# Kernel optimization log

Measured on AMD Instinct MI355X. Metric: run time of the kernel, lower is better.

Reference implementation:

```python
import jax, jax.numpy as jnp
import numpy as np

EMBED_DIM = 1024
NUM_HEADS = 16
HEAD_DIM = EMBED_DIM // NUM_HEADS
ROPE_BASE = 10000.0


def rotate_half(x):
    d = x.shape[-1] // 2
    x1, x2 = x[..., :d], x[..., d:]
    return jnp.concatenate((-x2, x1), axis=-1)


def setup_inputs() -> dict:
    key = jax.random.key(0)
    k_x, k_wqkv, k_bqkv, k_wo, k_bo = jax.random.split(key, 5)
    C = EMBED_DIM
    x = jax.random.normal(k_x, (4, 2048, C), dtype=jnp.float32)
    s = 1.0 / np.sqrt(C)
    W_qkv = jax.random.uniform(k_wqkv, (C, 3 * C), minval=-s, maxval=s, dtype=jnp.float32)
    b_qkv = jax.random.uniform(k_bqkv, (3 * C,), minval=-s, maxval=s, dtype=jnp.float32)
    W_out = jax.random.uniform(k_wo, (C, C), minval=-s, maxval=s, dtype=jnp.float32)
    b_out = jax.random.uniform(k_bo, (C,), minval=-s, maxval=s, dtype=jnp.float32)
    return {"x": x, "W_qkv": W_qkv, "b_qkv": b_qkv, "W_out": W_out, "b_out": b_out}


def reference(x, W_qkv, b_qkv, W_out, b_out):
    B, T, C = x.shape
    H, Dh = NUM_HEADS, HEAD_DIM
    # fused QKV projection: [B,T,3C] -> [3,B,H,T,Dh]
    qkv = (x @ W_qkv + b_qkv).reshape(B, T, 3, H, Dh).transpose(2, 0, 3, 1, 4)
    q, k, v = qkv[0], qkv[1], qkv[2]
    # rotary embedding: freqs [T, Dh/2] -> emb [T, Dh]
    inv_freq = 1.0 / (ROPE_BASE ** (jnp.arange(0, Dh, 2, dtype=jnp.float32) / Dh))
    freqs = jnp.arange(T, dtype=jnp.float32)[:, None] * inv_freq[None, :]
    emb = jnp.concatenate((freqs, freqs), axis=-1)  # [T, Dh], broadcasts over B,H
    cos, sin = jnp.cos(emb), jnp.sin(emb)
    q = q * cos + rotate_half(q) * sin
    k = k * cos + rotate_half(k) * sin
    # full (non-causal) attention, manual softmax
    scale = 1.0 / np.sqrt(Dh)
    attn = jax.nn.softmax(jnp.einsum("bhqd,bhkd->bhqk", q, k) * scale, axis=-1)
    out = jnp.einsum("bhqk,bhkd->bhqd", attn, v)  # [B,H,T,Dh]
    out = out.transpose(0, 2, 1, 3).reshape(B, T, C)
    return out @ W_out + b_out
```

## Files before the change

### kernel.cpp

```cpp
#include <hip/hip_runtime.h>
#include <math.h>

#define T_SEQ 2048
#define CDIM  1024
#define NH    16
#define DHD   64
#define BATCH 4
#define MROWS (BATCH * T_SEQ)
#define BHN   (BATCH * NH)

typedef _Float16 f16;
typedef __attribute__((ext_vector_type(8))) _Float16 f16x8;
typedef __attribute__((ext_vector_type(4))) _Float16 f16x4;
typedef __attribute__((ext_vector_type(2))) _Float16 f16x2;
typedef __attribute__((ext_vector_type(2))) __fp16 fp16x2;
typedef __attribute__((ext_vector_type(4))) float f32x4;

__device__ __forceinline__ float fast_exp2(float x) {
#if __has_builtin(__builtin_amdgcn_exp2f)
    return __builtin_amdgcn_exp2f(x);
#else
    return exp2f(x);
#endif
}

__device__ __forceinline__ float fast_rcp(float x) {
#if __has_builtin(__builtin_amdgcn_rcpf)
    return __builtin_amdgcn_rcpf(x);
#else
    return 1.0f / x;
#endif
}

__device__ __forceinline__ f16x2 cvt_pk_f16(float a, float b) {
    fp16x2 r = __builtin_amdgcn_cvt_pkrtz(a, b);
    return __builtin_bit_cast(f16x2, r);
}

__device__ __forceinline__ void gl_lds16(const f16* g, f16* l) {
    __builtin_amdgcn_global_load_lds(
        (const __attribute__((address_space(1))) void*)(g),
        (__attribute__((address_space(3))) void*)(l),
        16, 0, 0);
}

__global__ void rope_tables_kernel(float* __restrict__ ctab, float* __restrict__ stab)
{
    int idx = blockIdx.x * 256 + threadIdx.x;
    int t = idx >> 5, i = idx & 31;
    double inv = pow(10000.0, -(double)(2 * i) / 64.0);
    double a = (double)t * inv;
    ctab[idx] = (float)cos(a);
    stab[idx] = (float)sin(a);
}

__global__ __launch_bounds__(256) void xcvt_kernel(
    const float* __restrict__ X, f16* __restrict__ Xf)
{
    int idx = blockIdx.x * 256 + threadIdx.x;
    const float4* src = (const float4*)X + (size_t)idx * 2;
    float4 a = src[0], b = src[1];
    f16x8 o;
    o[0] = (f16)a.x; o[1] = (f16)a.y; o[2] = (f16)a.z; o[3] = (f16)a.w;
    o[4] = (f16)b.x; o[5] = (f16)b.y; o[6] = (f16)b.z; o[7] = (f16)b.w;
    *((f16x8*)Xf + idx) = o;
}

__global__ __launch_bounds__(64) void wcvt_kernel(
    const float* __restrict__ Wq, const float* __restrict__ Wo,
    f16* __restrict__ Wqt, f16* __restrict__ Wot)
{
    int lane = threadIdx.x;
    int k0 = blockIdx.x * 8;
    int ny = blockIdx.y;
    const float* W;
    f16* Wt;
    int N, n;
    if (ny < 48) { W = Wq; Wt = Wqt; N = 3072; n = ny * 64 + lane; }
    else         { W = Wo; Wt = Wot; N = 1024; n = (ny - 48) * 64 + lane; }
    f16x8 o;
#pragma unroll
    for (int j = 0; j < 8; j++) o[j] = (f16)W[(size_t)(k0 + j) * N + n];
    *(f16x8*)(Wt + (size_t)n * CDIM + k0) = o;
}

#define GEMM_MAINLOOP(Aimg, Bimg, M0, N0)                                         \
    __shared__ f16 As[128][64], Bs[128][64];                                      \
    const int tid = threadIdx.x, wave = tid >> 6, lane = tid & 63;                \
    const int l16 = lane & 15, quad = lane >> 4;                                  \
    const int wm = wave >> 1, wn = wave & 1;                                      \
    f32x4 acc[4][4];                                                              \
    _Pragma("unroll") for (int i = 0; i < 4; i++)                                 \
        _Pragma("unroll") for (int j = 0; j < 4; j++)                             \
            acc[i][j] = (f32x4){0.f, 0.f, 0.f, 0.f};                              \
    const f16* sbase = (wave < 2) ? (Aimg) : (Bimg);                              \
    f16* lbase = ((wave < 2) ? &As[0][0] : &Bs[0][0]) + (wave & 1) * 4096;        \
    const size_t srow0 = ((wave < 2) ? (size_t)(M0) : (size_t)(N0)) + (wave & 1) * 64; \
    const int srow = lane >> 3, schunk = lane & 7;                                \
    const int gchunk = (schunk ^ srow) << 3;         \
    for (int k0 = 0; k0 < CDIM; k0 += 64) {                                       \
        _Pragma("unroll") for (int it = 0; it < 8; it++)                          \
            gl_lds16(sbase + (srow0 + it * 8 + srow) * CDIM + k0 + gchunk,        \
                     lbase + it * 512);                                           \
        __syncthreads();                                                          \
        _Pragma("unroll") for (int ks = 0; ks < 2; ks++) {                        \
            f16x8 fa[4], fb[4];                                                   \
            _Pragma("unroll") for (int mi = 0; mi < 4; mi++)                      \
                fa[mi] = *(const f16x8*)                                          \
                    &As[wm * 64 + mi * 16 + l16][((ks * 4 + quad) ^ (l16 & 7)) << 3]; \
            _Pragma("unroll") for (int ni = 0; ni < 4; ni++)                      \
                fb[ni] = *(const f16x8*)                                          \
                    &Bs[wn * 64 + ni * 16 + l16][((ks * 4 + quad) ^ (l16 & 7)) << 3]; \
            _Pragma("unroll") for (int mi = 0; mi < 4; mi++)                      \
                _Pragma("unroll") for (int ni = 0; ni < 4; ni++)                  \
                    acc[mi][ni] = __builtin_amdgcn_mfma_f32_16x16x32_f16(         \
                        fa[mi], fb[ni], acc[mi][ni], 0, 0, 0);                    \
        }                                                                         \
        __syncthreads();                                                          \
    }

__global__ __launch_bounds__(256) void qkv_gemm_kernel(
    const f16* __restrict__ Xf, const f16* __restrict__ Wt,
    const float* __restrict__ bias,
    const float* __restrict__ ctab, const float* __restrict__ stab,
    f16* __restrict__ qf, f16* __restrict__ kf, f16* __restrict__ vtb)
{
    const int m0 = blockIdx.x * 128;
    const int n0 = blockIdx.y * 128;
    GEMM_MAINLOOP(Xf, Wt, m0, n0)

    const int ncol0 = n0 + wn * 64;
    const int w = ncol0 >> 10;
    const int h = (ncol0 >> 6) & 15;
    const int b = m0 >> 11;
    const int trow0 = (m0 & 2047) + wm * 64 + quad * 4;
    float bia[4];
#pragma unroll
    for (int ni = 0; ni < 4; ni++) bia[ni] = bias[ncol0 + ni * 16 + l16];

    if (w < 2) {
        f16* oq = w ? kf : qf;
        const float sc = w ? 1.0f : 0.18033688011112042f;
#pragma unroll
        for (int mi = 0; mi < 4; mi++) {
#pragma unroll
            for (int i = 0; i < 4; i++) {
                int t = trow0 + mi * 16 + i;
                size_t rowoff = ((size_t)(b * NH + h) * T_SEQ + t) * DHD;
#pragma unroll
                for (int np = 0; np < 2; np++) {
                    int d = np * 16 + l16;
                    float v0 = acc[mi][np][i] + bia[np];
                    float v1 = acc[mi][np + 2][i] + bia[np + 2];
                    float c = ctab[(t << 5) + d];
                    float s = stab[(t << 5) + d];
                    oq[rowoff + d]      = (f16)((v0 * c - v1 * s) * sc);
                    oq[rowoff + d + 32] = (f16)((v1 * c + v0 * s) * sc);
                }
            }
        }
    } else {
#pragma unroll
        for (int mi = 0; mi < 4; mi++) {
            const int tb = trow0 + mi * 16;
#pragma unroll
            for (int ni = 0; ni < 4; ni++) {
                const int d = ni * 16 + l16;
                f16x4 pv;
#pragma unroll
                for (int i = 0; i < 4; i++) pv[i] = (f16)(acc[mi][ni][i] + bia[ni]);
                *(f16x4*)(vtb + ((size_t)(b * NH + h) * DHD + d) * T_SEQ + tb) = pv;
            }
        }
    }
}

__global__ __launch_bounds__(256, 4) void attn_kernel(
    const f16* __restrict__ qf, const f16* __restrict__ kf,
    const f16* __restrict__ vt, f16* __restrict__ ab)
{
    __shared__ f16 Kb[2][64][64];
    __shared__ f16 Vb[2][64][64];
    __shared__ f16 Pb[4][32][32];

    const int tid  = threadIdx.x;
    const int wave = tid >> 6, lane = tid & 63;
    const int l16  = lane & 15, quad = lane >> 4;

    const int flat = blockIdx.x + (blockIdx.y << 4);
    const int swz  = (flat & 7) * 128 + (flat >> 3);
    const int qt = swz & 15;
    const int bh = swz >> 4;
    const int q0 = qt * 128 + wave * 32;

    const f16* kbase = kf + (size_t)bh * T_SEQ * DHD;
    const f16* vbase = vt + (size_t)bh * DHD * T_SEQ;

    f16x8 qfr[2][2];
#pragma unroll
    for (int qs = 0; qs < 2; qs++) {
        const f16* qrow = qf + ((size_t)bh * T_SEQ + q0 + qs * 16 + l16) * DHD;
        qfr[qs][0] = *(const f16x8*)(qrow + quad * 8);
        qfr[qs][1] = *(const f16x8*)(qrow + 32 + quad * 8);
    }

    f32x4 o[2][4];
    f32x4 lacc[2];
#pragma unroll
    for (int qs = 0; qs < 2; qs++) {
        lacc[qs] = (f32x4){0.f, 0.f, 0.f, 0.f};
#pragma unroll
        for (int dt = 0; dt < 4; dt++) o[qs][dt] = (f32x4){0.f, 0.f, 0.f, 0.f};
    }
    f16x8 ones;
#pragma unroll
    for (int j = 0; j < 8; j++) ones[j] = (f16)1.0f;

    const int srow = tid >> 3;
    const int scw  = tid & 7;
    const int scol = scw << 3;
    const int swzc = (scw ^ (srow & 7)) << 3;

    const int prot = l16 & 14;

    const f16* kp = kbase + (size_t)srow * DHD + scol;
    const f16* vp = vbase + (size_t)srow * T_SEQ + scol;

    f16x8 kreg[2], vreg[2];
#pragma unroll
    for (int r = 0; r < 2; r++) {
        kreg[r] = *(const f16x8*)(kp + (size_t)(r * 32) * DHD);
        vreg[r] = *(const f16x8*)(vp + (size_t)(r * 32) * T_SEQ);
    }
#pragma unroll
    for (int r = 0; r < 2; r++) {
        *(f16x8*)&Kb[0][srow + r * 32][swzc] = kreg[r];
        *(f16x8*)&Vb[0][srow + r * 32][swzc] = vreg[r];
    }
    const f16* kq = kp + 64 * DHD;
    const f16* vq = vp + 64;
    __syncthreads();

    for (int kt = 0; kt < 32; kt++) {
        const int buf = kt & 1;
        if (kt < 31) {
#pragma unroll
            for (int r = 0; r < 2; r++) {
                kreg[r] = *(const f16x8*)(kq + (size_t)(r * 32) * DHD);
                vreg[r] = *(const f16x8*)(vq + (size_t)(r * 32) * T_SEQ);
            }
            kq += 64 * DHD;
            vq += 64;
        }

#pragma unroll
        for (int half = 0; half < 2; half++) {
            f32x4 sc[2][2];
#pragma unroll
            for (int k2 = 0; k2 < 2; k2++)
#pragma unroll
                for (int qs = 0; qs < 2; qs++) sc[k2][qs] = (f32x4){0.f, 0.f, 0.f, 0.f};
            __builtin_amdgcn_s_setprio(1);
#pragma unroll
            for (int k2 = 0; k2 < 2; k2++) {
                const int keyt = half * 2 + k2;
#pragma unroll
                for (int ks = 0; ks < 2; ks++) {
                    const int kc = ((ks * 4 + quad) ^ (l16 & 7)) << 3;
                    f16x8 kfr = *(const f16x8*)&Kb[buf][keyt * 16 + l16][kc];
#pragma unroll
                    for (int qs = 0; qs < 2; qs++)
                        sc[k2][qs] = __builtin_amdgcn_mfma_f32_16x16x32_f16(
                            kfr, qfr[qs][ks], sc[k2][qs], 0, 0, 0);
                }
            }
            __builtin_amdgcn_s_setprio(0);
#pragma unroll
            for (int k2 = 0; k2 < 2; k2++) {
#pragma unroll
                for (int qs = 0; qs < 2; qs++) {
                    f16x2 pa = cvt_pk_f16(
                        fast_exp2(sc[k2][qs][0]), fast_exp2(sc[k2][qs][1]));
                    f16x2 pb = cvt_pk_f16(
                        fast_exp2(sc[k2][qs][2]), fast_exp2(sc[k2][qs][3]));
                    f16x4 pv;
                    ((f16x2*)&pv)[0] = pa;
                    ((f16x2*)&pv)[1] = pb;
                    const int pc = (((k2 << 3) + (quad << 1) + prot) & 15) << 1;
                    *(f16x4*)&Pb[wave][qs * 16 + l16][pc] = pv;
                }
            }
            const int pr0 = (((quad << 2)     + prot) & 15) << 1;
            const int pr1 = (((quad << 2) + 2 + prot) & 15) << 1;
            f16x8 pfr[2];
#pragma unroll
            for (int qs = 0; qs < 2; qs++) {
                f16x4 plo = *(const f16x4*)&Pb[wave][qs * 16 + l16][pr0];
                f16x4 phi = *(const f16x4*)&Pb[wave][qs * 16 + l16][pr1];
                f16x8 pf;
                pf[0] = plo[0]; pf[1] = plo[1]; pf[2] = plo[2]; pf[3] = plo[3];
                pf[4] = phi[0]; pf[5] = phi[1]; pf[6] = phi[2]; pf[7] = phi[3];
                pfr[qs] = pf;
            }
            __builtin_amdgcn_s_setprio(1);
#pragma unroll
            for (int qs = 0; qs < 2; qs++)
                lacc[qs] = __builtin_amdgcn_mfma_f32_16x16x32_f16(
                    pfr[qs], ones, lacc[qs], 0, 0, 0);
#pragma unroll
            for (int dt = 0; dt < 4; dt++) {
                const int vc = ((half * 4 + quad) ^ (l16 & 7)) << 3;
                f16x8 vfr = *(const f16x8*)&Vb[buf][dt * 16 + l16][vc];
#pragma unroll
                for (int qs = 0; qs < 2; qs++)
                    o[qs][dt] = __builtin_amdgcn_mfma_f32_16x16x32_f16(
                        pfr[qs], vfr, o[qs][dt], 0, 0, 0);
            }
            __builtin_amdgcn_s_setprio(0);
        }

        if (kt < 31) {
#pragma unroll
            for (int r = 0; r < 2; r++) {
                *(f16x8*)&Kb[buf ^ 1][srow + r * 32][swzc] = kreg[r];
                *(f16x8*)&Vb[buf ^ 1][srow + r * 32][swzc] = vreg[r];
            }
        }
        __syncthreads();
    }

    const int b = bh >> 4, h = bh & 15;
#pragma unroll
    for (int qs = 0; qs < 2; qs++) {
#pragma unroll
        for (int i = 0; i < 4; i++) {
            float iv = fast_rcp(lacc[qs][i]);
            int m = b * T_SEQ + qt * 128 + wave * 32 + qs * 16 + quad * 4 + i;
#pragma unroll
            for (int dt = 0; dt < 4; dt++)
                ab[(size_t)m * CDIM + h * 64 + dt * 16 + l16] = (f16)(o[qs][dt][i] * iv);
        }
    }
}

__global__ __launch_bounds__(256) void out_gemm_kernel(
    const f16* __restrict__ Ab, const f16* __restrict__ Wt,
    const float* __restrict__ bias, float* __restrict__ out)
{
    const int m0 = blockIdx.x * 128;
    const int n0 = blockIdx.y * 128;
    GEMM_MAINLOOP(Ab, Wt, m0, n0)

    const int ncol0 = n0 + wn * 64;
    float bia[4];
#pragma unroll
    for (int ni = 0; ni < 4; ni++) bia[ni] = bias[ncol0 + ni * 16 + l16];
#pragma unroll
    for (int mi = 0; mi < 4; mi++) {
#pragma unroll
        for (int i = 0; i < 4; i++) {
            int m = m0 + wm * 64 + mi * 16 + quad * 4 + i;
#pragma unroll
            for (int ni = 0; ni < 4; ni++)
                out[(size_t)m * CDIM + ncol0 + ni * 16 + l16] = acc[mi][ni][i] + bia[ni];
        }
    }
}

extern "C" void kernel_launch(void* const* d_in, const int* in_sizes, int n_in,
                              void* d_out, int out_size, void* d_ws, size_t ws_size,
                              hipStream_t stream)
{
    const float* x    = (const float*)d_in[0];
    const float* Wqkv = (const float*)d_in[1];
    const float* bqkv = (const float*)d_in[2];
    const float* Wout = (const float*)d_in[3];
    const float* bout = (const float*)d_in[4];
    float* out = (float*)d_out;

    const size_t XSZ  = (size_t)MROWS * CDIM;
    const size_t WQSZ = (size_t)3072 * CDIM;
    const size_t WOSZ = (size_t)CDIM * CDIM;
    const size_t QSZ  = (size_t)BHN * T_SEQ * DHD;

    char* p = (char*)d_ws;
    f16* Xf  = (f16*)p; p += XSZ * 2;
    f16* Wqt = (f16*)p; p += WQSZ * 2;
    f16* Wot = (f16*)p; p += WOSZ * 2;
    f16* qf  = (f16*)p; p += QSZ * 2;
    f16* kf  = (f16*)p; p += QSZ * 2;
    f16* vtb = (f16*)p; p += QSZ * 2;
    f16* ab  = (f16*)p; p += QSZ * 2;
    float* ctab = (float*)p; p += T_SEQ * 32 * 4;
    float* stab = (float*)p; p += T_SEQ * 32 * 4;

    rope_tables_kernel<<<256, 256, 0, stream>>>(ctab, stab);
    xcvt_kernel<<<(int)(XSZ / 8 / 256), 256, 0, stream>>>(x, Xf);
    wcvt_kernel<<<dim3(128, 64), 64, 0, stream>>>(Wqkv, Wout, Wqt, Wot);
    qkv_gemm_kernel<<<dim3(64, 24), 256, 0, stream>>>(
        Xf, Wqt, bqkv, ctab, stab, qf, kf, vtb);
    attn_kernel<<<dim3(16, BHN), 256, 0, stream>>>(qf, kf, vtb, ab);
    out_gemm_kernel<<<dim3(64, 8), 256, 0, stream>>>(ab, Wot, bout, out);
}
```

Baseline: 281.2 us.

## Merge prep kernels, use direct global-to-LDS loads and register-resident P in attention

Folds the three preprocessing kernels (rope tables, x conversion, weight transpose) into one launch to cut launch overhead. In attention, K/V tiles are now staged with global_load_lds straight into swizzled LDS instead of going through registers. The P tile is no longer round-tripped through shared memory: the score-MFMA output layout is fed directly into 16x16x16 MFMAs for both the PV product and the row sums. This removes LDS traffic and a barrier but doubles the MFMA instruction count with the smaller-K variant, and relies on the async LDS loads being complete at the __syncthreads.

```diff
diff --git a/kernel.cpp b/kernel.cpp
--- a/kernel.cpp
+++ b/kernel.cpp
@@ -44,44 +44,43 @@
         16, 0, 0);
 }
 
-__global__ void rope_tables_kernel(float* __restrict__ ctab, float* __restrict__ stab)
-{
-    int idx = blockIdx.x * 256 + threadIdx.x;
-    int t = idx >> 5, i = idx & 31;
-    double inv = pow(10000.0, -(double)(2 * i) / 64.0);
-    double a = (double)t * inv;
-    ctab[idx] = (float)cos(a);
-    stab[idx] = (float)sin(a);
-}
-
-__global__ __launch_bounds__(256) void xcvt_kernel(
-    const float* __restrict__ X, f16* __restrict__ Xf)
-{
-    int idx = blockIdx.x * 256 + threadIdx.x;
-    const float4* src = (const float4*)X + (size_t)idx * 2;
-    float4 a = src[0], b = src[1];
-    f16x8 o;
-    o[0] = (f16)a.x; o[1] = (f16)a.y; o[2] = (f16)a.z; o[3] = (f16)a.w;
-    o[4] = (f16)b.x; o[5] = (f16)b.y; o[6] = (f16)b.z; o[7] = (f16)b.w;
-    *((f16x8*)Xf + idx) = o;
-}
-
-__global__ __launch_bounds__(64) void wcvt_kernel(
+__global__ __launch_bounds__(256) void prep_kernel(
+    const float* __restrict__ X, f16* __restrict__ Xf,
     const float* __restrict__ Wq, const float* __restrict__ Wo,
-    f16* __restrict__ Wqt, f16* __restrict__ Wot)
-{
-    int lane = threadIdx.x;
-    int k0 = blockIdx.x * 8;
-    int ny = blockIdx.y;
-    const float* W;
-    f16* Wt;
-    int N, n;
-    if (ny < 48) { W = Wq; Wt = Wqt; N = 3072; n = ny * 64 + lane; }
-    else         { W = Wo; Wt = Wot; N = 1024; n = (ny - 48) * 64 + lane; }
-    f16x8 o;
-#pragma unroll
-    for (int j = 0; j < 8; j++) o[j] = (f16)W[(size_t)(k0 + j) * N + n];
-    *(f16x8*)(Wt + (size_t)n * CDIM + k0) = o;
+    f16* __restrict__ Wqt, f16* __restrict__ Wot,
+    float* __restrict__ ctab, float* __restrict__ stab)
+{
+    const int bx = blockIdx.x;
+    if (bx < 256) {
+        int idx = bx * 256 + threadIdx.x;
+        int t = idx >> 5, i = idx & 31;
+        double inv = pow(10000.0, -(double)(2 * i) / 64.0);
+        double a = (double)t * inv;
+        ctab[idx] = (float)cos(a);
+        stab[idx] = (float)sin(a);
+    } else if (bx < 4352) {
+        int idx = (bx - 256) * 256 + threadIdx.x;
+        const float4* src = (const float4*)X + (size_t)idx * 2;
+        float4 a = src[0], b = src[1];
+        f16x8 o;
+        o[0] = (f16)a.x; o[1] = (f16)a.y; o[2] = (f16)a.z; o[3] = (f16)a.w;
+        o[4] = (f16)b.x; o[5] = (f16)b.y; o[6] = (f16)b.z; o[7] = (f16)b.w;
+        *((f16x8*)Xf + idx) = o;
+    } else {
+        const int sub = threadIdx.x >> 6, lane = threadIdx.x & 63;
+        const int id = (bx - 4352) * 4 + sub;
+        const int k0 = (id & 127) * 8;
+        const int ny = id >> 7;
+        const float* W;
+        f16* Wt;
+        int N, n;
+        if (ny < 48) { W = Wq; Wt = Wqt; N = 3072; n = ny * 64 + lane; }
+        else         { W = Wo; Wt = Wot; N = 1024; n = (ny - 48) * 64 + lane; }
+        f16x8 o;
+#pragma unroll
+        for (int j = 0; j < 8; j++) o[j] = (f16)W[(size_t)(k0 + j) * N + n];
+        *(f16x8*)(Wt + (size_t)n * CDIM + k0) = o;
+    }
 }
 
 #define GEMM_MAINLOOP(Aimg, Bimg, M0, N0)                                         \
@@ -181,7 +180,6 @@
 {
     __shared__ f16 Kb[2][64][64];
     __shared__ f16 Vb[2][64][64];
-    __shared__ f16 Pb[4][32][32];
 
     const int tid  = threadIdx.x;
     const int wave = tid >> 6, lane = tid & 63;
@@ -212,46 +210,32 @@
 #pragma unroll
         for (int dt = 0; dt < 4; dt++) o[qs][dt] = (f32x4){0.f, 0.f, 0.f, 0.f};
     }
-    f16x8 ones;
-#pragma unroll
-    for (int j = 0; j < 8; j++) ones[j] = (f16)1.0f;
+    f16x4 ones4;
+#pragma unroll
+    for (int j = 0; j < 4; j++) ones4[j] = (f16)1.0f;
 
     const int srow = tid >> 3;
-    const int scw  = tid & 7;
-    const int scol = scw << 3;
-    const int swzc = (scw ^ (srow & 7)) << 3;
-
-    const int prot = l16 & 14;
-
-    const f16* kp = kbase + (size_t)srow * DHD + scol;
-    const f16* vp = vbase + (size_t)srow * T_SEQ + scol;
-
-    f16x8 kreg[2], vreg[2];
-#pragma unroll
-    for (int r = 0; r < 2; r++) {
-        kreg[r] = *(const f16x8*)(kp + (size_t)(r * 32) * DHD);
-        vreg[r] = *(const f16x8*)(vp + (size_t)(r * 32) * T_SEQ);
-    }
-#pragma unroll
-    for (int r = 0; r < 2; r++) {
-        *(f16x8*)&Kb[0][srow + r * 32][swzc] = kreg[r];
-        *(f16x8*)&Vb[0][srow + r * 32][swzc] = vreg[r];
-    }
-    const f16* kq = kp + 64 * DHD;
-    const f16* vq = vp + 64;
+    const int schunk = tid & 7;
+    const int gcol = (schunk ^ (srow & 7)) << 3;
+
+#define STAGE(t, b)                                                               \
+    {                                                                             \
+        const f16* kg = kbase + ((size_t)(t) * 64 + srow) * DHD + gcol;           \
+        const f16* vg = vbase + (size_t)srow * T_SEQ + (t) * 64 + gcol;           \
+        f16* kl = &Kb[b][wave * 8][0];                                            \
+        f16* vl = &Vb[b][wave * 8][0];                                            \
+        gl_lds16(kg, kl);                                                         \
+        gl_lds16(kg + 32 * DHD, kl + 32 * 64);                                    \
+        gl_lds16(vg, vl);                                                         \
+        gl_lds16(vg + (size_t)32 * T_SEQ, vl + 32 * 64);                          \
+    }
+
+    STAGE(0, 0)
     __syncthreads();
 
     for (int kt = 0; kt < 32; kt++) {
         const int buf = kt & 1;
-        if (kt < 31) {
-#pragma unroll
-            for (int r = 0; r < 2; r++) {
-                kreg[r] = *(const f16x8*)(kq + (size_t)(r * 32) * DHD);
-                vreg[r] = *(const f16x8*)(vq + (size_t)(r * 32) * T_SEQ);
-            }
-            kq += 64 * DHD;
-            vq += 64;
-        }
+        if (kt < 31) STAGE(kt + 1, buf ^ 1)
 
 #pragma unroll
         for (int half = 0; half < 2; half++) {
@@ -275,59 +259,43 @@
                 }
             }
             __builtin_amdgcn_s_setprio(0);
+            f16x4 pp[2][2];
 #pragma unroll
             for (int k2 = 0; k2 < 2; k2++) {
 #pragma unroll
                 for (int qs = 0; qs < 2; qs++) {
-                    f16x2 pa = cvt_pk_f16(
+                    ((f16x2*)&pp[k2][qs])[0] = cvt_pk_f16(
                         fast_exp2(sc[k2][qs][0]), fast_exp2(sc[k2][qs][1]));
-                    f16x2 pb = cvt_pk_f16(
+                    ((f16x2*)&pp[k2][qs])[1] = cvt_pk_f16(
                         fast_exp2(sc[k2][qs][2]), fast_exp2(sc[k2][qs][3]));
-                    f16x4 pv;
-                    ((f16x2*)&pv)[0] = pa;
-                    ((f16x2*)&pv)[1] = pb;
-                    const int pc = (((k2 << 3) + (quad << 1) + prot) & 15) << 1;
-                    *(f16x4*)&Pb[wave][qs * 16 + l16][pc] = pv;
                 }
             }
-            const int pr0 = (((quad << 2)     + prot) & 15) << 1;
-            const int pr1 = (((quad << 2) + 2 + prot) & 15) << 1;
-            f16x8 pfr[2];
-#pragma unroll
-            for (int qs = 0; qs < 2; qs++) {
-                f16x4 plo = *(const f16x4*)&Pb[wave][qs * 16 + l16][pr0];
-                f16x4 phi = *(const f16x4*)&Pb[wave][qs * 16 + l16][pr1];
-                f16x8 pf;
-                pf[0] = plo[0]; pf[1] = plo[1]; pf[2] = plo[2]; pf[3] = plo[3];
-                pf[4] = phi[0]; pf[5] = phi[1]; pf[6] = phi[2]; pf[7] = phi[3];
-                pfr[qs] = pf;
-            }
             __builtin_amdgcn_s_setprio(1);
 #pragma unroll
             for (int qs = 0; qs < 2; qs++)
-                lacc[qs] = __builtin_amdgcn_mfma_f32_16x16x32_f16(
-                    pfr[qs], ones, lacc[qs], 0, 0, 0);
+#pragma unroll
+                for (int k2 = 0; k2 < 2; k2++)
+                    lacc[qs] = __builtin_amdgcn_mfma_f32_16x16x16f16(
+                        pp[k2][qs], ones4, lacc[qs], 0, 0, 0);
 #pragma unroll
             for (int dt = 0; dt < 4; dt++) {
-                const int vc = ((half * 4 + quad) ^ (l16 & 7)) << 3;
-                f16x8 vfr = *(const f16x8*)&Vb[buf][dt * 16 + l16][vc];
-#pragma unroll
-                for (int qs = 0; qs < 2; qs++)
-                    o[qs][dt] = __builtin_amdgcn_mfma_f32_16x16x32_f16(
-                        pfr[qs], vfr, o[qs][dt], 0, 0, 0);
+#pragma unroll
+                for (int c = 0; c < 2; c++) {
+                    const int vc = ((half * 4 + c * 2 + (quad >> 1)) ^ (l16 & 7)) * 8
+                                 + (quad & 1) * 4;
+                    f16x4 vfr = *(const f16x4*)&Vb[buf][dt * 16 + l16][vc];
+#pragma unroll
+                    for (int qs = 0; qs < 2; qs++)
+                        o[qs][dt] = __builtin_amdgcn_mfma_f32_16x16x16f16(
+                            pp[c][qs], vfr, o[qs][dt], 0, 0, 0);
+                }
             }
             __builtin_amdgcn_s_setprio(0);
         }
 
-        if (kt < 31) {
-#pragma unroll
-            for (int r = 0; r < 2; r++) {
-                *(f16x8*)&Kb[buf ^ 1][srow + r * 32][swzc] = kreg[r];
-                *(f16x8*)&Vb[buf ^ 1][srow + r * 32][swzc] = vreg[r];
-            }
-        }
-        __syncthreads();
-    }
+        if (kt < 31) __syncthreads();
+    }
+#undef STAGE
 
     const int b = bh >> 4, h = bh & 15;
 #pragma unroll
@@ -394,9 +362,7 @@
     float* ctab = (float*)p; p += T_SEQ * 32 * 4;
     float* stab = (float*)p; p += T_SEQ * 32 * 4;
 
-    rope_tables_kernel<<<256, 256, 0, stream>>>(ctab, stab);
-    xcvt_kernel<<<(int)(XSZ / 8 / 256), 256, 0, stream>>>(x, Xf);
-    wcvt_kernel<<<dim3(128, 64), 64, 0, stream>>>(Wqkv, Wout, Wqt, Wot);
+    prep_kernel<<<6400, 256, 0, stream>>>(x, Xf, Wqkv, Wout, Wqt, Wot, ctab, stab);
     qkv_gemm_kernel<<<dim3(64, 24), 256, 0, stream>>>(
         Xf, Wqt, bqkv, ctab, stab, qf, kf, vtb);
     attn_kernel<<<dim3(16, BHN), 256, 0, stream>>>(qf, kf, vtb, ab);
```

Result: no change. 276.4 us (-1.7%).
